# Kernel optimization log

Hardware: AMD Instinct MI355X
Metric: run time of the kernel (lower is better)

The kernel has to match this reference:

```python
import jax, jax.numpy as jnp
import numpy as np

T, N, NH, H, R, E = 6, 50000, 128, 4, 2, 800000
D = NH // H


def _pos_enc(d, t):
    # matches HTHGNLayer TempAttention.generate_positional_encoding
    k = np.arange(0, d, 2)
    div = np.exp(k * -np.log(100000.0) / d)
    pos = np.arange(1, t + 1)[:, None].astype(np.float64)
    pe = np.zeros((t, d), dtype=np.float32)
    pe[:, 0::2] = np.sin(pos * div)
    pe[:, 1::2] = np.cos(pos * div)
    return jnp.asarray(pe)


def setup_inputs() -> dict:
    key = jax.random.key(0)
    ks = jax.random.split(key, 16)
    s = 1.0 / np.sqrt(NH)  # keep activations / attention logits well-scaled
    inp = {
        "x": jax.random.normal(ks[0], (T, N, NH), jnp.float32),
        "src": jax.random.randint(ks[1], (R, E), 0, N, jnp.int32),
        "dst": jax.random.randint(ks[2], (R, E), 0, N, jnp.int32),
        "gat_wsrc": jax.random.normal(ks[3], (R, NH, NH), jnp.float32) * s,
        "gat_wdst": jax.random.normal(ks[4], (R, NH, NH), jnp.float32) * s,
        "gat_attn": jax.random.normal(ks[5], (R, H, D), jnp.float32) * s,
        "gat_bias": jnp.zeros((R, NH), jnp.float32),
        "h_bias": jnp.zeros((NH,), jnp.float32),
        "sem_w1": jax.random.normal(ks[6], (NH, NH), jnp.float32) * s,
        "sem_b1": jnp.zeros((NH,), jnp.float32),
        "sem_w2": jax.random.normal(ks[7], (NH,), jnp.float32) * s,
        "proj_w": jax.random.normal(ks[8], (NH, NH), jnp.float32) * s,
        "proj_b": jnp.zeros((NH,), jnp.float32),
        "qw": jax.random.normal(ks[9], (NH, NH), jnp.float32) * s,
        "kw": jax.random.normal(ks[10], (NH, NH), jnp.float32) * s,
        "vw": jax.random.normal(ks[11], (NH, NH), jnp.float32) * s,
        "fc_w": jax.random.normal(ks[12], (NH, NH), jnp.float32) * s,
        "fc_b": jnp.zeros((NH,), jnp.float32),
        "res_w": jax.random.normal(ks[13], (NH, NH), jnp.float32) * s,
        "res_b": jnp.zeros((NH,), jnp.float32),
        "res_alpha": jax.random.normal(ks[14], (1,), jnp.float32),
        "ln_gamma": jnp.ones((NH,), jnp.float32),
        "ln_beta": jnp.zeros((NH,), jnp.float32),
    }
    return inp


def _gatv2_rel(xt, s_, d_, wsrc, wdst, attn, bias):
    # one relation, one timestep: DGL GATv2Conv (share_weights=False, slope 0.2)
    fs = (xt @ wsrc).reshape(N, H, D)  # fc_src
    fd = (xt @ wdst).reshape(N, H, D)  # fc_dst
    e = jax.nn.leaky_relu(fs[s_] + fd[d_], 0.2)           # [E,H,D]
    sc = jnp.einsum('ehd,hd->eh', e, attn)                # [E,H]
    m = jax.ops.segment_max(sc, d_, num_segments=N)       # edge softmax per dst
    ex = jnp.exp(sc - m[d_])
    den = jax.ops.segment_sum(ex, d_, num_segments=N)
    alpha = ex / den[d_]
    out = jax.ops.segment_sum(alpha[:, :, None] * fs[s_], d_, num_segments=N)
    return out + bias.reshape(1, H, D)                    # [N,H,D]


def reference(x, src, dst, gat_wsrc, gat_wdst, gat_attn, gat_bias, h_bias,
              sem_w1, sem_b1, sem_w2, proj_w, proj_b, qw, kw, vw, fc_w, fc_b,
              res_w, res_b, res_alpha, ln_gamma, ln_beta):
    gat_all = jax.vmap(_gatv2_rel, in_axes=(None, 0, 0, 0, 0, 0, 0))
    inter = []
    for t in range(T):  # fixed small time window
        hr = gat_all(x[t], src, dst, gat_wsrc, gat_wdst, gat_attn, gat_bias)  # [R,N,H,D]
        h = jnp.transpose(hr, (1, 0, 2, 3)).reshape(N, R, NH)  # stack + flatten heads
        # semantic attention over relations (_rel_agg)
        w = jnp.tanh(h @ sem_w1 + sem_b1) @ sem_w2             # [N,R]
        beta = jax.nn.softmax(w.mean(0), axis=0)               # [R]
        hsem = jax.nn.relu(jnp.einsum('r,nrd->nd', beta, h))
        inter.append(jax.nn.relu(hsem + h_bias))               # _apply: bias + relu
    inter = jnp.stack(inter, 0)                                # [T,N,NH]
    # temporal self-attention (TempAttention, no 1/sqrt(d) scaling -- faithful)
    pe = _pos_enc(NH, T)
    xt = jnp.transpose(inter, (1, 0, 2))                       # [N,T,NH]
    hh = xt @ proj_w + proj_b + pe
    q, k, v = hh @ qw, hh @ kw, hh @ vw
    sc = jax.nn.softmax(jnp.einsum('ntd,nsd->nts', q, k), axis=-1)
    ho = jax.nn.relu(jnp.einsum('nts,nsd->ntd', sc, v) @ fc_w + fc_b)
    ho = jnp.transpose(ho, (1, 0, 2))                          # [T,N,NH]
    # gated residual + LayerNorm
    a = jax.nn.sigmoid(res_alpha)[0]
    out = ho * a + (x @ res_w + res_b) * (1.0 - a)
    mu = out.mean(-1, keepdims=True)
    var = out.var(-1, keepdims=True)
    return (out - mu) / jnp.sqrt(var + 1e-5) * ln_gamma + ln_beta
```

## Files before the change

### kernel.cpp

```cpp
#include <hip/hip_runtime.h>
#include <math.h>

#define T_  6
#define N_  50000
#define NH_ 128
#define R_  2
#define E_  800000
#define SEMW_BLOCKS ((2*N_ + 127)/128)
#define NCHUNK 49

typedef __attribute__((ext_vector_type(8))) short bf16x8;
typedef __attribute__((ext_vector_type(4))) float f32x4;

__device__ inline unsigned short f2b(float f) {
    union { float f; unsigned int u; } v; v.f = f;
    unsigned int u = v.u;
    unsigned int r = (u + 0x7FFFu + ((u >> 16) & 1u)) >> 16;
    return (unsigned short)r;
}
__device__ inline float b2f(unsigned short h) {
    union { unsigned int u; float f; } v; v.u = ((unsigned int)h) << 16;
    return v.f;
}
__device__ inline void gload16(const void* g, void* l) {
    __builtin_amdgcn_global_load_lds((const __attribute__((address_space(1))) void*)g,
                                     (__attribute__((address_space(3))) void*)l, 16, 0, 0);
}

__global__ void hist_kernel(const int* __restrict__ dst, int* __restrict__ counts) {
    int j = blockIdx.x * blockDim.x + threadIdx.x;
    if (j < R_ * E_) atomicAdd(&counts[(j / E_) * N_ + dst[j]], 1);
}

__global__ __launch_bounds__(1024) void scan1_kernel(const int* __restrict__ counts,
                                                     int* __restrict__ lexcl,
                                                     int* __restrict__ csums) {
    int r = blockIdx.y, c = blockIdx.x;
    int i = c * 1024 + threadIdx.x;
    int v = (i < N_) ? counts[r * N_ + i] : 0;
    __shared__ int sm[1024];
    sm[threadIdx.x] = v;
    __syncthreads();
    for (int off = 1; off < 1024; off <<= 1) {
        int t = 0;
        if (threadIdx.x >= off) t = sm[threadIdx.x - off];
        __syncthreads();
        sm[threadIdx.x] += t;
        __syncthreads();
    }
    if (i < N_) lexcl[r * N_ + i] = sm[threadIdx.x] - v;
    if (threadIdx.x == 1023) csums[r * 64 + c] = sm[1023];
}

__global__ void scan2_kernel(int* __restrict__ csums, int* __restrict__ offsets) {
    int r = threadIdx.x >> 6, l = threadIdx.x & 63;
    if (r < R_) {
        int v = (l < NCHUNK) ? csums[r * 64 + l] : 0;
        int s = v;
        for (int off = 1; off < 64; off <<= 1) {
            int t = __shfl_up(s, off);
            if (l >= off) s += t;
        }
        if (l < NCHUNK) csums[r * 64 + l] = s - v;
        if (l == NCHUNK - 1) offsets[r * (N_ + 1) + N_] = s;
    }
}

__global__ __launch_bounds__(1024) void scan3_kernel(const int* __restrict__ lexcl,
                                                     const int* __restrict__ csums,
                                                     int* __restrict__ offsets,
                                                     int* __restrict__ cursor) {
    int r = blockIdx.y;
    int i = blockIdx.x * 1024 + threadIdx.x;
    if (i < N_) {
        int o = lexcl[r * N_ + i] + csums[r * 64 + blockIdx.x];
        offsets[r * (N_ + 1) + i] = o;
        cursor[r * N_ + i] = o;
    }
}

__global__ void scatter_kernel(const int* __restrict__ src, const int* __restrict__ dst,
                               int* __restrict__ cursor, int* __restrict__ srcs_sorted) {
    int j = blockIdx.x * blockDim.x + threadIdx.x;
    if (j < R_ * E_) {
        int r = j / E_;
        int pos = atomicAdd(&cursor[r * N_ + dst[j]], 1);
        srcs_sorted[(size_t)r * E_ + pos] = src[j] << 8;
    }
}

__global__ void pe_kernel(float* __restrict__ pe) {
    int c = threadIdx.x;
    int k = c & ~1;
    double div = exp((double)k * (-log(100000.0) / 128.0));
    for (int t = 0; t < T_; t++) {
        double pos = (double)(t + 1);
        double v = (c & 1) ? cos(pos * div) : sin(pos * div);
        pe[t * NH_ + c] = (float)v;
    }
}

struct CvtArgs {
    const float* s[6];
    unsigned short* d[6];
};
__global__ void cvt_wt_kernel(CvtArgs a) {
    int y = blockIdx.y, n = blockIdx.x, k = threadIdx.x;
    a.d[y][n * 128 + k] = f2b(a.s[y][k * 128 + n]);
}

__global__ void build_m_kernel(const float* __restrict__ qw, const float* __restrict__ kw,
                               const float* __restrict__ vw, const float* __restrict__ fcw,
                               float* __restrict__ Mu, float* __restrict__ Mwv) {
    int y = blockIdx.y, c = blockIdx.x, f = threadIdx.x;
    float s = 0.f;
    if (y == 0) {
        for (int d = 0; d < 128; d++) s += kw[f * 128 + d] * qw[c * 128 + d];
        Mu[c * 128 + f] = s;
    } else {
        for (int d = 0; d < 128; d++) s += vw[f * 128 + d] * fcw[d * 128 + c];
        Mwv[c * 128 + f] = s;
    }
}

__global__ void fold_w_kernel(const float* __restrict__ proj, const float* __restrict__ Mu,
                              const float* __restrict__ Mwv, unsigned short* __restrict__ wt_hh,
                              unsigned short* __restrict__ wt_pu, unsigned short* __restrict__ wt_pwv) {
    int y = blockIdx.y, c = blockIdx.x, k = threadIdx.x;
    if (y == 0) { wt_hh[c * 128 + k] = f2b(proj[k * 128 + c]); return; }
    const float* M = (y == 1) ? Mu : Mwv;
    float s = 0.f;
    for (int f = 0; f < 128; f++) s += proj[k * 128 + f] * M[c * 128 + f];
    ((y == 1) ? wt_pu : wt_pwv)[c * 128 + k] = f2b(s);
}

__global__ void fold_c_kernel(const float* __restrict__ proj_b, const float* __restrict__ pe,
                              const float* __restrict__ Mu, const float* __restrict__ Mwv,
                              const float* __restrict__ res_b, float* __restrict__ cbuf) {
    int t = blockIdx.x, c = threadIdx.x;
    cbuf[0 * 768 + t * 128 + c] = proj_b[c] + pe[t * 128 + c];
    float s1 = 0.f, s2 = 0.f;
    for (int f = 0; f < 128; f++) {
        float b = proj_b[f] + pe[t * 128 + f];
        s1 += b * Mu[c * 128 + f];
        s2 += b * Mwv[c * 128 + f];
    }
    cbuf[1 * 768 + t * 128 + c] = s1;
    cbuf[2 * 768 + t * 128 + c] = s2;
    cbuf[3 * 768 + t * 128 + c] = res_b[c];
}

struct MArgs {
    const void* A;
    const void* Axb;
    const unsigned short* W0; const unsigned short* W1;
    const unsigned short* W2; const unsigned short* W3;
    unsigned short* C0; unsigned short* C1; unsigned short* C2; unsigned short* C3;
    const float* cb;
    long row0;
    int  M;
};

template <int EPI>
__global__ __launch_bounds__(256) void mgemm_kernel(MArgs g) {
    __shared__ __align__(16) char As[128 * 256];
    __shared__ __align__(16) char Bs[128 * 256];
    int tid = threadIdx.x;
    int lane = tid & 63;
    int wbase = tid & ~63;
    int brow0 = blockIdx.x * 128;
    const unsigned short* Ws[4] = {g.W0, g.W1, g.W2, g.W3};
    unsigned short* Cs[4] = {g.C0, g.C1, g.C2, g.C3};

    auto stageAsync = [&](const char* Sbase, char* L, bool clampRows) {
        int Mm1 = g.M - 1;
#pragma unroll
        for (int i = 0; i < 8; i++) {
            int c0 = wbase + i * 256;
            int cl = c0 + lane;
            int row = cl >> 4;
            int sb = ((cl & 15) << 4) ^ ((row & 7) << 4);
            long srow = clampRows ? (long)min(brow0 + row, Mm1) : (long)row;
            gload16(Sbase + srow * 256 + sb, L + (size_t)c0 * 16);
        }
    };
    auto stageA_f32 = [&](const float* Abase, bool m1) {
#pragma unroll
        for (int i = 0; i < 8; i++) {
            int c = tid + i * 256;
            int row = c >> 4;
            int cb = (c & 15) << 4;
            int scb = cb ^ ((row & 7) << 4);
            int grow = brow0 + row;
            uint4 av = make_uint4(0u, 0u, 0u, 0u);
            if (grow < g.M) {
                long ar;
                if (!m1) ar = grow;
                else { long gg = g.row0 + grow; long n = gg / 6, t = gg - n * 6; ar = t * (long)N_ + n; }
                const float* Af = Abase + ar * 128 + (cb >> 1);
                float4 x0 = *(const float4*)Af;
                float4 x1 = *(const float4*)(Af + 4);
                union { unsigned short s[8]; uint4 u; } o;
                o.s[0] = f2b(x0.x); o.s[1] = f2b(x0.y); o.s[2] = f2b(x0.z); o.s[3] = f2b(x0.w);
                o.s[4] = f2b(x1.x); o.s[5] = f2b(x1.y); o.s[6] = f2b(x1.z); o.s[7] = f2b(x1.w);
                av = o.u;
            }
            *(uint4*)(As + row * 256 + scb) = av;
        }
    };

    int w = tid >> 6, l = tid & 63;
    int l15 = l & 15, lg = l >> 4;

    if (EPI == 0) stageA_f32((const float*)g.A, false);
    else          stageAsync((const char*)g.A, As, true);

    for (int y = 0; y < 4; y++) {
        if (y > 0) __syncthreads();
        if (EPI == 3 && y == 3) stageA_f32((const float*)g.Axb, true);
        stageAsync((const char*)Ws[y], Bs, false);
        __syncthreads();

        f32x4 acc[2][8];
#pragma unroll
        for (int a = 0; a < 2; a++)
#pragma unroll
            for (int b = 0; b < 8; b++) acc[a][b] = (f32x4)(0.f);
#pragma unroll
        for (int ks = 0; ks < 4; ks++) {
            bf16x8 bf[8];
#pragma unroll
            for (int nt = 0; nt < 8; nt++) {
                int rn = nt * 16 + l15;
                int cbyte = (ks * 64 + lg * 16) ^ ((rn & 7) << 4);
                bf[nt] = *(const bf16x8*)(Bs + rn * 256 + cbyte);
            }
#pragma unroll
            for (int mt = 0; mt < 2; mt++) {
                int rm = w * 32 + mt * 16 + l15;
                int cbyte = (ks * 64 + lg * 16) ^ ((rm & 7) << 4);
                bf16x8 af = *(const bf16x8*)(As + rm * 256 + cbyte);
#pragma unroll
                for (int nt = 0; nt < 8; nt++)
                    acc[mt][nt] = __builtin_amdgcn_mfma_f32_16x16x32_bf16(af, bf[nt], acc[mt][nt], 0, 0, 0);
            }
        }
        unsigned short* C = Cs[y];
#pragma unroll
        for (int mt = 0; mt < 2; mt++) {
#pragma unroll
            for (int r = 0; r < 4; r++) {
                int row = w * 32 + mt * 16 + lg * 4 + r;
                int grow = brow0 + row;
                if (grow >= g.M) continue;
                long t6 = 0;
                if (EPI == 3) t6 = (g.row0 + grow) % 6;
#pragma unroll
                for (int nt = 0; nt < 8; nt++) {
                    int col = nt * 16 + l15;
                    float v = acc[mt][nt][r];
                    if (EPI == 3) v += g.cb[y * 768 + t6 * 128 + col];
                    C[(size_t)grow * 128 + col] = f2b(v);
                }
            }
        }
    }
}

__global__ __launch_bounds__(256) void semw_kernel(const unsigned short* __restrict__ Abase,
                                                   const unsigned short* __restrict__ Wt,
                                                   const float* __restrict__ b1,
                                                   const float* __restrict__ w2,
                                                   float* __restrict__ partials) {
    __shared__ __align__(16) char As[128 * 256];
    __shared__ __align__(16) char Bs[128 * 256];
    __shared__ float bs[2];
    int tid = threadIdx.x;
    if (tid < 2) bs[tid] = 0.f;
    int lane = tid & 63;
    int wbase = tid & ~63;
    int tl = blockIdx.y;
    const char* A = (const char*)(Abase + (size_t)tl * N_ * 256);
    const int M = 2 * N_;
    int brow0 = blockIdx.x * 128;
#pragma unroll
    for (int i = 0; i < 8; i++) {
        int c0 = wbase + i * 256;
        int cl = c0 + lane;
        int row = cl >> 4;
        int sb = ((cl & 15) << 4) ^ ((row & 7) << 4);
        gload16((const char*)Wt + (long)row * 256 + sb, Bs + (size_t)c0 * 16);
        long srow = min(brow0 + row, M - 1);
        gload16(A + srow * 256 + sb, As + (size_t)c0 * 16);
    }
    __syncthreads();
    int w = tid >> 6, l = tid & 63;
    int l15 = l & 15, lg = l >> 4;
    f32x4 acc[2][8];
#pragma unroll
    for (int a = 0; a < 2; a++)
#pragma unroll
        for (int b = 0; b < 8; b++) acc[a][b] = (f32x4)(0.f);
#pragma unroll
    for (int ks = 0; ks < 4; ks++) {
        bf16x8 bf[8];
#pragma unroll
        for (int nt = 0; nt < 8; nt++) {
            int rn = nt * 16 + l15;
            int cbyte = (ks * 64 + lg * 16) ^ ((rn & 7) << 4);
            bf[nt] = *(const bf16x8*)(Bs + rn * 256 + cbyte);
        }
#pragma unroll
        for (int mt = 0; mt < 2; mt++) {
            int rm = w * 32 + mt * 16 + l15;
            int cbyte = (ks * 64 + lg * 16) ^ ((rm & 7) << 4);
            bf16x8 af = *(const bf16x8*)(As + rm * 256 + cbyte);
#pragma unroll
            for (int nt = 0; nt < 8; nt++)
                acc[mt][nt] = __builtin_amdgcn_mfma_f32_16x16x32_bf16(af, bf[nt], acc[mt][nt], 0, 0, 0);
        }
    }
#pragma unroll
    for (int mt = 0; mt < 2; mt++) {
#pragma unroll
        for (int r = 0; r < 4; r++) {
            int row = w * 32 + mt * 16 + lg * 4 + r;
            int grow = brow0 + row;
            float s = 0.f;
#pragma unroll
            for (int nt = 0; nt < 8; nt++) {
                int col = nt * 16 + l15;
                s += tanhf(acc[mt][nt][r] + b1[col]) * w2[col];
            }
#pragma unroll
            for (int mask = 1; mask <= 8; mask <<= 1) s += __shfl_xor(s, mask);
            if (l15 == 0 && grow < M) atomicAdd(&bs[grow & 1], s);
        }
    }
    __syncthreads();
    if (tid < 2) partials[((size_t)tl * SEMW_BLOCKS + blockIdx.x) * 2 + tid] = bs[tid];
}

__global__ __launch_bounds__(512) void beta_kernel(const float* __restrict__ partials,
                                                   float* __restrict__ beta2) {
    int t = blockIdx.x;
    const float* p = partials + (size_t)t * SEMW_BLOCKS * 2;
    float s0 = 0.f, s1 = 0.f;
    for (int i = threadIdx.x; i < SEMW_BLOCKS; i += 512) { s0 += p[i * 2]; s1 += p[i * 2 + 1]; }
#pragma unroll
    for (int mask = 1; mask <= 32; mask <<= 1) { s0 += __shfl_xor(s0, mask); s1 += __shfl_xor(s1, mask); }
    __shared__ float w0[8], w1[8];
    int w = threadIdx.x >> 6;
    if ((threadIdx.x & 63) == 0) { w0[w] = s0; w1[w] = s1; }
    __syncthreads();
    if (threadIdx.x == 0) {
        float t0 = 0.f, t1 = 0.f;
        for (int i = 0; i < 8; i++) { t0 += w0[i]; t1 += w1[i]; }
        float m0 = t0 / (float)N_, m1 = t1 / (float)N_;
        float mx = fmaxf(m0, m1);
        float e0 = __expf(m0 - mx), e1 = __expf(m1 - mx);
        float inv = 1.f / (e0 + e1);
        beta2[t * 2] = e0 * inv; beta2[t * 2 + 1] = e1 * inv;
    }
}

__global__ __launch_bounds__(256) void gat_edge_kernel(const unsigned short* __restrict__ R0,
                                                       const int* __restrict__ offsets,
                                                       const int* __restrict__ srcs_sorted,
                                                       const float* __restrict__ gat_attn,
                                                       const float* __restrict__ gat_bias,
                                                       unsigned short* __restrict__ hbuf, int TB) {
    int y = blockIdx.x >> 10;
    int bid = blockIdx.x & 1023;
    int r = y & 1, tl = y >> 1;
    const char* fsb = (const char*)(R0 + ((size_t)(2 * r) * TB + tl) * N_ * 128);
    const unsigned short* fd = R0 + ((size_t)(2 * r + 1) * TB + tl) * N_ * 128;
    unsigned short* hout = hbuf + (size_t)tl * N_ * 256;
    const int* offs = offsets + r * (N_ + 1);
    const int* srcs = srcs_sorted + (size_t)r * E_;
    int lane = threadIdx.x & 63;
    int q = lane >> 4, l16 = lane & 15;
    int c0 = l16 * 8;
    const char* fsc = fsb + c0 * 2;
    int wid = (bid * blockDim.x + threadIdx.x) >> 6;
    int nw = (1024 * blockDim.x) >> 6;
    float4 a0 = *(const float4*)(gat_attn + r * 128 + c0);
    float4 a1 = *(const float4*)(gat_attn + r * 128 + c0 + 4);
    float av[8] = {a0.x, a0.y, a0.z, a0.w, a1.x, a1.y, a1.z, a1.w};
    float4 bb0 = *(const float4*)(gat_bias + r * 128 + c0);
    float4 bb1 = *(const float4*)(gat_bias + r * 128 + c0 + 4);
    float bv[8] = {bb0.x, bb0.y, bb0.z, bb0.w, bb1.x, bb1.y, bb1.z, bb1.w};

    for (int gidx = wid; gidx < N_ / 4; gidx += nw) {
        int n = gidx * 4 + q;
        uint4 fdp = *(const uint4*)(fd + (size_t)n * 128 + c0);
        const unsigned int* fdu = (const unsigned int*)&fdp;
        float fdv[8];
#pragma unroll
        for (int j = 0; j < 8; j++)
            fdv[j] = (j & 1) ? b2f((unsigned short)(fdu[j >> 1] >> 16)) : b2f((unsigned short)fdu[j >> 1]);
        int e0 = offs[n], e1 = offs[n + 1];
        int deg = e1 - e0;
        int m = deg;
        m = max(m, __shfl_xor(m, 16));
        m = max(m, __shfl_xor(m, 32));
        float den = 0.f;
        float acc[8];
#pragma unroll
        for (int j = 0; j < 8; j++) acc[j] = 0.f;

        uint4 fp = make_uint4(0u, 0u, 0u, 0u);
        if (deg > 0) fp = *(const uint4*)(fsc + srcs[e0]);
        for (int i = 0; i < m; i++) {
            uint4 nxt = make_uint4(0u, 0u, 0u, 0u);
            if (i + 1 < deg) nxt = *(const uint4*)(fsc + srcs[e0 + i + 1]);
            const unsigned int* fu = (const unsigned int*)&fp;
            float f[8];
            float vlin = 0.f, vabs = 0.f;
#pragma unroll
            for (int j = 0; j < 8; j++) {
                f[j] = (j & 1) ? b2f((unsigned short)(fu[j >> 1] >> 16)) : b2f((unsigned short)fu[j >> 1]);
                float t = f[j] + fdv[j];
                vlin = fmaf(av[j], t, vlin);
                vabs = fmaf(av[j], fabsf(t), vabs);
            }
            float v = fmaf(0.4f, vabs, 0.6f * vlin);
            v += __int_as_float(__builtin_amdgcn_ds_swizzle(__float_as_int(v), 0x041F));
            v += __int_as_float(__builtin_amdgcn_ds_swizzle(__float_as_int(v), 0x081F));
            float p = (i < deg) ? __expf(v) : 0.f;
            den += p;
#pragma unroll
            for (int j = 0; j < 8; j++) acc[j] = fmaf(p, f[j], acc[j]);
            fp = nxt;
        }
        float inv = (deg > 0) ? 1.f / den : 0.f;
        union { unsigned short s[8]; uint4 u; } o;
#pragma unroll
        for (int j = 0; j < 8; j++) o.s[j] = f2b(fmaf(acc[j], inv, bv[j]));
        *(uint4*)(hout + (size_t)(n * 2 + r) * 128 + c0) = o.u;
    }
}

__global__ void hsem_kernel(const unsigned short* __restrict__ hbuf, const float* __restrict__ beta2,
                            const float* __restrict__ h_bias, unsigned short* __restrict__ inter,
                            int tbase) {
    int idx = blockIdx.x * blockDim.x + threadIdx.x;
    if (idx >= N_ * 16) return;
    int tl = blockIdx.y;
    int t = tbase + tl;
    const unsigned short* h = hbuf + (size_t)tl * N_ * 256;
    int n = idx >> 4, c8 = (idx & 15) * 8;
    float b0 = beta2[tl * 2], b1 = beta2[tl * 2 + 1];
    uint4 x0 = *(const uint4*)(h + (size_t)n * 256 + c8);
    uint4 x1 = *(const uint4*)(h + (size_t)n * 256 + 128 + c8);
    const unsigned int* p0 = (const unsigned int*)&x0;
    const unsigned int* p1 = (const unsigned int*)&x1;
    float4 hb0 = *(const float4*)(h_bias + c8);
    float4 hb1 = *(const float4*)(h_bias + c8 + 4);
    float hbv[8] = {hb0.x, hb0.y, hb0.z, hb0.w, hb1.x, hb1.y, hb1.z, hb1.w};
    union { unsigned short s[8]; uint4 u; } o;
#pragma unroll
    for (int i = 0; i < 8; i++) {
        unsigned short s0 = (i & 1) ? (unsigned short)(p0[i >> 1] >> 16) : (unsigned short)p0[i >> 1];
        unsigned short s1 = (i & 1) ? (unsigned short)(p1[i >> 1] >> 16) : (unsigned short)p1[i >> 1];
        float z = fmaxf(fmaxf(b0 * b2f(s0) + b1 * b2f(s1), 0.f) + hbv[i], 0.f);
        o.s[i] = f2b(z);
    }
    *(uint4*)(inter + ((size_t)n * 6 + t) * 128 + c8) = o.u;
}

__global__ __launch_bounds__(256) void temporal_kernel(const unsigned short* __restrict__ hh,
                                                       const unsigned short* __restrict__ uu,
                                                       const unsigned short* __restrict__ wvv,
                                                       const unsigned short* __restrict__ rv,
                                                       const float* __restrict__ fc_b,
                                                       const float* __restrict__ res_alpha,
                                                       const float* __restrict__ ln_g,
                                                       const float* __restrict__ ln_b,
                                                       float* __restrict__ out, long n0, int nNodes) {
    int lane = threadIdx.x & 63;
    int wid = (blockIdx.x * blockDim.x + threadIdx.x) >> 6;
    if (wid >= nNodes) return;
    long n = n0 + wid;
    size_t base = (size_t)wid * 6 * 128 + 2 * lane;
    float h2[6][2], u2[6][2], wv2[6][2], rv2[6][2];
#pragma unroll
    for (int t = 0; t < 6; t++) {
        unsigned int hp = *(const unsigned int*)(hh + base + t * 128);
        h2[t][0] = b2f((unsigned short)hp); h2[t][1] = b2f((unsigned short)(hp >> 16));
        unsigned int up = *(const unsigned int*)(uu + base + t * 128);
        u2[t][0] = b2f((unsigned short)up); u2[t][1] = b2f((unsigned short)(up >> 16));
        unsigned int wp = *(const unsigned int*)(wvv + base + t * 128);
        wv2[t][0] = b2f((unsigned short)wp); wv2[t][1] = b2f((unsigned short)(wp >> 16));
        unsigned int rp = *(const unsigned int*)(rv + base + t * 128);
        rv2[t][0] = b2f((unsigned short)rp); rv2[t][1] = b2f((unsigned short)(rp >> 16));
    }
    float sc[6][6];
#pragma unroll
    for (int t = 0; t < 6; t++)
#pragma unroll
        for (int s = 0; s < 6; s++)
            sc[t][s] = h2[t][0] * u2[s][0] + h2[t][1] * u2[s][1];
#pragma unroll
    for (int mask = 1; mask <= 32; mask <<= 1)
#pragma unroll
        for (int t = 0; t < 6; t++)
#pragma unroll
            for (int s = 0; s < 6; s++)
                sc[t][s] += __shfl_xor(sc[t][s], mask);

    float a = 1.f / (1.f + __expf(-res_alpha[0]));
    float2 fb = ((const float2*)fc_b)[lane];
    float2 lg = ((const float2*)ln_g)[lane];
    float2 lb = ((const float2*)ln_b)[lane];
#pragma unroll
    for (int t = 0; t < 6; t++) {
        float mx = sc[t][0];
#pragma unroll
        for (int s = 1; s < 6; s++) mx = fmaxf(mx, sc[t][s]);
        float p[6]; float den = 0.f;
#pragma unroll
        for (int s = 0; s < 6; s++) { p[s] = __expf(sc[t][s] - mx); den += p[s]; }
        float inv = 1.f / den;
        float ox = 0.f, oy = 0.f;
#pragma unroll
        for (int s = 0; s < 6; s++) { ox += p[s] * wv2[s][0]; oy += p[s] * wv2[s][1]; }
        ox = fmaxf(ox * inv + fb.x, 0.f);
        oy = fmaxf(oy * inv + fb.y, 0.f);
        ox = ox * a + rv2[t][0] * (1.f - a);
        oy = oy * a + rv2[t][1] * (1.f - a);
        float s1 = ox + oy, s2 = ox * ox + oy * oy;
#pragma unroll
        for (int mask = 1; mask <= 32; mask <<= 1) {
            s1 += __shfl_xor(s1, mask);
            s2 += __shfl_xor(s2, mask);
        }
        float mu = s1 * (1.f / 128.f);
        float var = s2 * (1.f / 128.f) - mu * mu;
        float rs = rsqrtf(var + 1e-5f);
        float2 o;
        o.x = (ox - mu) * rs * lg.x + lb.x;
        o.y = (oy - mu) * rs * lg.y + lb.y;
        ((float2*)(out + ((size_t)t * N_ + n) * 128))[lane] = o;
    }
}

extern "C" void kernel_launch(void* const* d_in, const int* in_sizes, int n_in,
                              void* d_out, int out_size, void* d_ws, size_t ws_size,
                              hipStream_t stream) {
    const float* x        = (const float*)d_in[0];
    const int*   src      = (const int*)d_in[1];
    const int*   dst      = (const int*)d_in[2];
    const float* gat_wsrc = (const float*)d_in[3];
    const float* gat_wdst = (const float*)d_in[4];
    const float* gat_attn = (const float*)d_in[5];
    const float* gat_bias = (const float*)d_in[6];
    const float* h_bias   = (const float*)d_in[7];
    const float* sem_w1   = (const float*)d_in[8];
    const float* sem_b1   = (const float*)d_in[9];
    const float* sem_w2   = (const float*)d_in[10];
    const float* proj_w   = (const float*)d_in[11];
    const float* proj_b   = (const float*)d_in[12];
    const float* qw       = (const float*)d_in[13];
    const float* kw       = (const float*)d_in[14];
    const float* vw       = (const float*)d_in[15];
    const float* fc_w     = (const float*)d_in[16];
    const float* fc_b     = (const float*)d_in[17];
    const float* res_w    = (const float*)d_in[18];
    const float* res_b    = (const float*)d_in[19];
    const float* res_alpha= (const float*)d_in[20];
    const float* ln_g     = (const float*)d_in[21];
    const float* ln_b     = (const float*)d_in[22];
    (void)in_sizes; (void)n_in; (void)out_size;

    int TB = (ws_size >= (size_t)500 * 1024 * 1024) ? 6 : 2;
    int CH = (TB == 6) ? N_ : 12500;

    char* ws = (char*)d_ws;
    size_t off = 0;
    auto alloc = [&](size_t bytes) -> void* {
        void* p = ws + off;
        off += (bytes + 255) & ~(size_t)255;
        return p;
    };
    int*   counts      = (int*)alloc((size_t)R_ * N_ * 4);
    int*   offsets     = (int*)alloc((size_t)R_ * (N_ + 1) * 4);
    int*   cursor      = (int*)alloc((size_t)R_ * N_ * 4);
    int*   srcs_sorted = (int*)alloc((size_t)R_ * E_ * 4);
    int*   lexcl       = (int*)alloc((size_t)R_ * N_ * 4);
    int*   csums       = (int*)alloc((size_t)R_ * 64 * 4);
    float* pe          = (float*)alloc(T_ * NH_ * 4);
    float* partials    = (float*)alloc((size_t)T_ * SEMW_BLOCKS * 2 * 4);
    float* beta2       = (float*)alloc(T_ * 2 * 4);
    float* Mu          = (float*)alloc(16384 * 4);
    float* Mwv         = (float*)alloc(16384 * 4);
    float* cbuf        = (float*)alloc(4 * 768 * 4);
    unsigned short* wt_gs0  = (unsigned short*)alloc(16384 * 2);
    unsigned short* wt_gs1  = (unsigned short*)alloc(16384 * 2);
    unsigned short* wt_gd0  = (unsigned short*)alloc(16384 * 2);
    unsigned short* wt_gd1  = (unsigned short*)alloc(16384 * 2);
    unsigned short* wt_sem  = (unsigned short*)alloc(16384 * 2);
    unsigned short* wt_res  = (unsigned short*)alloc(16384 * 2);
    unsigned short* wt_hh   = (unsigned short*)alloc(16384 * 2);
    unsigned short* wt_pu   = (unsigned short*)alloc(16384 * 2);
    unsigned short* wt_pwv  = (unsigned short*)alloc(16384 * 2);
    unsigned short* inter   = (unsigned short*)alloc((size_t)N_ * T_ * 128 * 2);
    size_t Rgat = (size_t)4 * TB * N_ * 128 * 2;
    size_t Rtmp = (size_t)4 * CH * 6 * 128 * 2;
    unsigned short* R0      = (unsigned short*)alloc(Rgat > Rtmp ? Rgat : Rtmp);

    unsigned short* hbuf = (unsigned short*)d_out;

    hipMemsetAsync(counts, 0, (size_t)R_ * N_ * 4, stream);
    hist_kernel<<<(R_ * E_ + 255) / 256, 256, 0, stream>>>(dst, counts);
    scan1_kernel<<<dim3(NCHUNK, R_), 1024, 0, stream>>>(counts, lexcl, csums);
    scan2_kernel<<<1, 128, 0, stream>>>(csums, offsets);
    scan3_kernel<<<dim3(NCHUNK, R_), 1024, 0, stream>>>(lexcl, csums, offsets, cursor);
    scatter_kernel<<<(R_ * E_ + 255) / 256, 256, 0, stream>>>(src, dst, cursor, srcs_sorted);
    pe_kernel<<<1, 128, 0, stream>>>(pe);
    CvtArgs ca;
    ca.s[0] = gat_wsrc;         ca.d[0] = wt_gs0;
    ca.s[1] = gat_wsrc + 16384; ca.d[1] = wt_gs1;
    ca.s[2] = gat_wdst;         ca.d[2] = wt_gd0;
    ca.s[3] = gat_wdst + 16384; ca.d[3] = wt_gd1;
    ca.s[4] = sem_w1;           ca.d[4] = wt_sem;
    ca.s[5] = res_w;            ca.d[5] = wt_res;
    cvt_wt_kernel<<<dim3(128, 6), 128, 0, stream>>>(ca);
    build_m_kernel<<<dim3(128, 2), 128, 0, stream>>>(qw, kw, vw, fc_w, Mu, Mwv);
    fold_w_kernel<<<dim3(128, 3), 128, 0, stream>>>(proj_w, Mu, Mwv, wt_hh, wt_pu, wt_pwv);
    fold_c_kernel<<<6, 128, 0, stream>>>(proj_b, pe, Mu, Mwv, res_b, cbuf);

    size_t TBN = (size_t)TB * N_ * 128;
    for (int tg = 0; tg < T_ / TB; tg++) {
        int tbase = tg * TB;
        MArgs ga{};
        ga.A = (const void*)(x + (size_t)tbase * N_ * 128);
        ga.row0 = 0; ga.M = TB * N_;
        ga.W0 = wt_gs0; ga.C0 = R0;
        ga.W1 = wt_gd0; ga.C1 = R0 + TBN;
        ga.W2 = wt_gs1; ga.C2 = R0 + 2 * TBN;
        ga.W3 = wt_gd1; ga.C3 = R0 + 3 * TBN;
        mgemm_kernel<0><<<dim3((TB * N_ + 127) / 128, 1), 256, 0, stream>>>(ga);

        gat_edge_kernel<<<1024 * 2 * TB, 256, 0, stream>>>(R0, offsets, srcs_sorted,
                                                           gat_attn, gat_bias, hbuf, TB);

        semw_kernel<<<dim3(SEMW_BLOCKS, TB), 256, 0, stream>>>(hbuf, wt_sem, sem_b1, sem_w2,
                                                               partials + (size_t)tbase * SEMW_BLOCKS * 2);
        beta_kernel<<<TB, 512, 0, stream>>>(partials + (size_t)tbase * SEMW_BLOCKS * 2,
                                            beta2 + tbase * 2);
        hsem_kernel<<<dim3((N_ * 16 + 255) / 256, TB), 256, 0, stream>>>(hbuf, beta2 + tbase * 2,
                                                                         h_bias, inter, tbase);
    }

    for (int c = 0; c < N_ / CH; c++) {
        long n0 = (long)c * CH;
        long r0 = n0 * 6;
        int Mc = CH * 6;
        int nb = (Mc + 127) / 128;
        size_t MB = (size_t)Mc * 128;

        MArgs gt{};
        gt.A = (const void*)(inter + (size_t)r0 * 128);
        gt.Axb = (const void*)x;
        gt.row0 = r0; gt.M = Mc; gt.cb = cbuf;
        gt.W0 = wt_hh;  gt.C0 = R0;
        gt.W1 = wt_pu;  gt.C1 = R0 + MB;
        gt.W2 = wt_pwv; gt.C2 = R0 + 2 * MB;
        gt.W3 = wt_res; gt.C3 = R0 + 3 * MB;
        mgemm_kernel<3><<<dim3(nb, 1), 256, 0, stream>>>(gt);

        temporal_kernel<<<(CH + 3) / 4, 256, 0, stream>>>(R0, R0 + MB, R0 + 2 * MB, R0 + 3 * MB,
                                                          fc_b, res_alpha, ln_g, ln_b,
                                                          (float*)d_out, n0, CH);
    }
}
```

Measured before the change: 1.223 ms.

## Sort destination nodes by degree within windows to balance GAT edge wavefronts

Adds a per-window bitonic sort of destination nodes by in-degree, producing a permutation that gat_edge_kernel uses to group nodes of similar degree into the same wavefront. Each wavefront processes four nodes and loops to the maximum degree among them, so grouping similar degrees is meant to cut wasted iterations spent waiting on the highest-degree node. The cost is an extra small kernel, an indirect node lookup, padded slots that are skipped, and less contiguous access to fd and hbuf rows.

```diff
diff --git a/kernel.cpp b/kernel.cpp
--- a/kernel.cpp
+++ b/kernel.cpp
@@ -8,6 +8,8 @@
 #define E_  800000
 #define SEMW_BLOCKS ((2*N_ + 127)/128)
 #define NCHUNK 49
+#define NWIN  196
+#define NPAD  (NWIN*256)
 
 typedef __attribute__((ext_vector_type(8))) short bf16x8;
 typedef __attribute__((ext_vector_type(4))) float f32x4;
@@ -87,6 +89,37 @@
         int pos = atomicAdd(&cursor[r * N_ + dst[j]], 1);
         srcs_sorted[(size_t)r * E_ + pos] = src[j] << 8;
     }
+}
+
+__global__ __launch_bounds__(256) void wsort_kernel(const int* __restrict__ counts,
+                                                    int* __restrict__ perm) {
+    int r = blockIdx.y;
+    int w0 = blockIdx.x * 256;
+    int tid = threadIdx.x;
+    int n = w0 + tid;
+    int key;
+    if (n < N_) {
+        int d = counts[r * N_ + n]; d = d < 0x7FFE ? d : 0x7FFE;
+        key = (d << 16) | tid;
+    } else {
+        key = (0x7FFF << 16) | tid;
+    }
+    __shared__ int sk[256];
+    sk[tid] = key;
+    __syncthreads();
+    for (int k = 2; k <= 256; k <<= 1) {
+        for (int j = k >> 1; j > 0; j >>= 1) {
+            int ixj = tid ^ j;
+            if (ixj > tid) {
+                int a = sk[tid], b = sk[ixj];
+                bool asc = ((tid & k) == 0);
+                if ((a > b) == asc) { sk[tid] = b; sk[ixj] = a; }
+            }
+            __syncthreads();
+        }
+    }
+    int kk = sk[tid];
+    perm[r * NPAD + w0 + tid] = ((kk >> 16) == 0x7FFF) ? -1 : (w0 + (kk & 0xFFFF));
 }
 
 __global__ void pe_kernel(float* __restrict__ pe) {
@@ -367,6 +400,7 @@
 __global__ __launch_bounds__(256) void gat_edge_kernel(const unsigned short* __restrict__ R0,
                                                        const int* __restrict__ offsets,
                                                        const int* __restrict__ srcs_sorted,
+                                                       const int* __restrict__ perm,
                                                        const float* __restrict__ gat_attn,
                                                        const float* __restrict__ gat_bias,
                                                        unsigned short* __restrict__ hbuf, int TB) {
@@ -378,6 +412,7 @@
     unsigned short* hout = hbuf + (size_t)tl * N_ * 256;
     const int* offs = offsets + r * (N_ + 1);
     const int* srcs = srcs_sorted + (size_t)r * E_;
+    const int* pm = perm + r * NPAD;
     int lane = threadIdx.x & 63;
     int q = lane >> 4, l16 = lane & 15;
     int c0 = l16 * 8;
@@ -391,15 +426,19 @@
     float4 bb1 = *(const float4*)(gat_bias + r * 128 + c0 + 4);
     float bv[8] = {bb0.x, bb0.y, bb0.z, bb0.w, bb1.x, bb1.y, bb1.z, bb1.w};
 
-    for (int gidx = wid; gidx < N_ / 4; gidx += nw) {
-        int n = gidx * 4 + q;
-        uint4 fdp = *(const uint4*)(fd + (size_t)n * 128 + c0);
+    for (int gidx = wid; gidx < NPAD / 4; gidx += nw) {
+        int n = pm[gidx * 4 + q];
+        int e0 = 0, e1 = 0;
+        uint4 fdp = make_uint4(0u, 0u, 0u, 0u);
+        if (n >= 0) {
+            e0 = offs[n]; e1 = offs[n + 1];
+            fdp = *(const uint4*)(fd + (size_t)n * 128 + c0);
+        }
         const unsigned int* fdu = (const unsigned int*)&fdp;
         float fdv[8];
 #pragma unroll
         for (int j = 0; j < 8; j++)
             fdv[j] = (j & 1) ? b2f((unsigned short)(fdu[j >> 1] >> 16)) : b2f((unsigned short)fdu[j >> 1]);
-        int e0 = offs[n], e1 = offs[n + 1];
         int deg = e1 - e0;
         int m = deg;
         m = max(m, __shfl_xor(m, 16));
@@ -433,11 +472,13 @@
             for (int j = 0; j < 8; j++) acc[j] = fmaf(p, f[j], acc[j]);
             fp = nxt;
         }
-        float inv = (deg > 0) ? 1.f / den : 0.f;
-        union { unsigned short s[8]; uint4 u; } o;
-#pragma unroll
-        for (int j = 0; j < 8; j++) o.s[j] = f2b(fmaf(acc[j], inv, bv[j]));
-        *(uint4*)(hout + (size_t)(n * 2 + r) * 128 + c0) = o.u;
+        if (n >= 0) {
+            float inv = (deg > 0) ? 1.f / den : 0.f;
+            union { unsigned short s[8]; uint4 u; } o;
+#pragma unroll
+            for (int j = 0; j < 8; j++) o.s[j] = f2b(fmaf(acc[j], inv, bv[j]));
+            *(uint4*)(hout + (size_t)(n * 2 + r) * 128 + c0) = o.u;
+        }
     }
 }
 
@@ -589,6 +630,7 @@
     int*   srcs_sorted = (int*)alloc((size_t)R_ * E_ * 4);
     int*   lexcl       = (int*)alloc((size_t)R_ * N_ * 4);
     int*   csums       = (int*)alloc((size_t)R_ * 64 * 4);
+    int*   perm        = (int*)alloc((size_t)R_ * NPAD * 4);
     float* pe          = (float*)alloc(T_ * NH_ * 4);
     float* partials    = (float*)alloc((size_t)T_ * SEMW_BLOCKS * 2 * 4);
     float* beta2       = (float*)alloc(T_ * 2 * 4);
@@ -617,6 +659,7 @@
     scan2_kernel<<<1, 128, 0, stream>>>(csums, offsets);
     scan3_kernel<<<dim3(NCHUNK, R_), 1024, 0, stream>>>(lexcl, csums, offsets, cursor);
     scatter_kernel<<<(R_ * E_ + 255) / 256, 256, 0, stream>>>(src, dst, cursor, srcs_sorted);
+    wsort_kernel<<<dim3(NWIN, R_), 256, 0, stream>>>(counts, perm);
     pe_kernel<<<1, 128, 0, stream>>>(pe);
     CvtArgs ca;
     ca.s[0] = gat_wsrc;         ca.d[0] = wt_gs0;
@@ -642,7 +685,7 @@
         ga.W3 = wt_gd1; ga.C3 = R0 + 3 * TBN;
         mgemm_kernel<0><<<dim3((TB * N_ + 127) / 128, 1), 256, 0, stream>>>(ga);
 
-        gat_edge_kernel<<<1024 * 2 * TB, 256, 0, stream>>>(R0, offsets, srcs_sorted,
+        gat_edge_kernel<<<1024 * 2 * TB, 256, 0, stream>>>(R0, offsets, srcs_sorted, perm,
                                                            gat_attn, gat_bias, hbuf, TB);
 
         semw_kernel<<<dim3(SEMW_BLOCKS, TB), 256, 0, stream>>>(hbuf, wt_sem, sem_b1, sem_w2,
```

Result: slower. 1.288 ms (+5.3%).
